# Performance work log

Hardware: AMD Instinct MI355X
Metric: run time of the kernel (lower is better)

Reference implementation:

```python
import jax, jax.numpy as jnp
import numpy as np

B, TX, DA, DS, H = 64, 2048, 256, 256, 50

def setup_inputs() -> dict:
    key = jax.random.key(0)
    k1, k2, k3, k4 = jax.random.split(key, 4)
    a = jax.random.normal(k1, (B, TX, DA), dtype=jnp.float32)
    s = jax.random.normal(k2, (B, DS), dtype=jnp.float32)
    # Dense(50, relu) params on concat dim (DA+DS)
    W1 = jax.random.normal(k3, (DA + DS, H), dtype=jnp.float32) / np.sqrt(DA + DS)
    b1 = jnp.zeros((H,), dtype=jnp.float32)
    # Dense(1, tanh) params
    W2 = jax.random.normal(k4, (H, 1), dtype=jnp.float32) / np.sqrt(H)
    b2 = jnp.zeros((1,), dtype=jnp.float32)
    return {"a": a, "s": s, "W1": W1, "b1": b1, "W2": W2, "b2": b2}

def reference(a, s, W1, b1, W2, b2):
    # repeat s along time: [B, Tx, Ds]
    s_rep = jnp.broadcast_to(s[:, None, :], (a.shape[0], a.shape[1], s.shape[-1]))
    x = jnp.concatenate([a, s_rep], axis=-1)              # [B, Tx, Da+Ds]
    h = jax.nn.relu(jnp.einsum('btc,ch->bth', x, W1) + b1)  # [B, Tx, 50]
    e = jnp.tanh(jnp.einsum('bth,ho->bto', h, W2) + b2)     # [B, Tx, 1]
    alphas = jax.nn.softmax(e, axis=1)                     # softmax over time
    # Dot(axes=1): contract the time axis -> [B, 1, Da]
    context = jnp.einsum('bto,btd->bod', alphas, a)
    return context
```

## Files before the change

kernel.cpp:

```cpp
#include <hip/hip_runtime.h>

#define B_ 64
#define TX_ 2048
#define DA_ 256
#define DS_ 256
#define H_ 50

typedef __attribute__((ext_vector_type(4))) float f32x4;
typedef __attribute__((ext_vector_type(8))) short short8;

__device__ __forceinline__ unsigned short f2bf(float x) {
  unsigned int u = __builtin_bit_cast(unsigned int, x);
  u += 0x7FFFu + ((u >> 16) & 1u);
  return (unsigned short)(u >> 16);
}
__device__ __forceinline__ float bf2f(unsigned short h) {
  unsigned int u = ((unsigned int)h) << 16;
  return __builtin_bit_cast(float, u);
}

#define WS_NUM 0
#define WS_DEN 16384
#define WS_C   16448
#define WS_W2  20544
#define WS_B   20608

__global__ __launch_bounds__(256) void prep_kernel(
    const float* __restrict__ s, const float* __restrict__ W1,
    const float* __restrict__ b1, const float* __restrict__ W2,
    float* __restrict__ ws)
{
  const int b = blockIdx.x;
  const int t = threadIdx.x;
  float* num = ws + WS_NUM;
  float* den = ws + WS_DEN;
  float* cws = ws + WS_C;
  float* w2p = ws + WS_W2;
  unsigned short* wsB = (unsigned short*)(ws + WS_B);

  num[b * 256 + t] = 0.0f;
  if (t == 0) den[b] = 0.0f;

  {
    const int h4 = t >> 2, kq = t & 3;
    float cp = 0.0f;
    if (h4 < H_) {
      const float* srow = s + b * DS_;
      #pragma unroll 8
      for (int k = kq * 64; k < kq * 64 + 64; ++k)
        cp += srow[k] * W1[(size_t)(DA_ + k) * H_ + h4];
    }
    cp += __shfl_down(cp, 1);
    cp += __shfl_down(cp, 2);
    if (kq == 0) cws[b * 64 + h4] = (h4 < H_) ? (cp + b1[h4]) : 0.0f;
  }
  if (b == 0 && t < 64) w2p[t] = (t < H_) ? W2[t] : 0.0f;

  #pragma unroll
  for (int ii = 0; ii < 2; ++ii) {
    const int idx = (b * 256 + t) * 2 + ii;
    const int j = idx & 7;
    const int l = (idx >> 3) & 63;
    const int nt = (idx >> 9) & 3;
    const int term = (idx >> 11) & 1;
    const int c = idx >> 12;
    const int k = c * 32 + (l >> 4) * 8 + j;
    const int n = nt * 16 + (l & 15);
    const float wv = (n < H_) ? W1[(size_t)k * H_ + n] : 0.0f;
    const unsigned short hi = f2bf(wv);
    const unsigned short val = term == 0 ? hi : f2bf(wv - bf2f(hi));
    wsB[((size_t)((c * 2 + term) * 4 + nt)) * 512 + l * 8 + j] = val;
  }
}

__global__ __launch_bounds__(256) void fused_kernel(
    const float* __restrict__ a, const float* __restrict__ ws_f,
    const float* __restrict__ b2, float* __restrict__ num,
    float* __restrict__ den)
{
  __shared__ float tile[16384];
  __shared__ float w_sh[64];

  const int t = threadIdx.x;
  const int l = t & 63;
  const int w = __builtin_amdgcn_readfirstlane(t >> 6);
  const int blk = blockIdx.x;
  const int b = blk >> 5;
  const long R0 = (long)blk * 64;

  const float* cws = ws_f + WS_C;
  const float* w2p = ws_f + WS_W2;
  const unsigned short* wsB = (const unsigned short*)(ws_f + WS_B);

  float cv[4], w2v[4];
  #pragma unroll
  for (int nt = 0; nt < 4; ++nt) {
    const int n = nt * 16 + (l & 15);
    cv[nt] = cws[b * 64 + n];
    w2v[nt] = w2p[n];
  }
  const float b2v = b2[0];

  #define STAGE(c)                                                             \
    {                                                                          \
      _Pragma("unroll")                                                        \
      for (int i = 0; i < 2; ++i) {                                            \
        const int slot = w * 2 + i;                                            \
        const int row = slot * 8 + (l >> 3);                                   \
        const long gbyte = (R0 + row) * 1024 + (c) * 128 +                     \
                           (((l & 7) ^ ((l >> 3) & 7)) * 16);                  \
        __builtin_amdgcn_global_load_lds(                                      \
            (const __attribute__((address_space(1))) void*)((const char*)a +   \
                                                            gbyte),            \
            (__attribute__((address_space(3))) void*)&tile[(c)*2048 +          \
                                                           slot * 256],        \
            16, 0, 0);                                                         \
      }                                                                        \
    }

  STAGE(0);
  STAGE(1);

  short8 Bh[2][4], Bl[2][4];
  {
    const short8* Bp = (const short8*)wsB;
    #pragma unroll
    for (int nt = 0; nt < 4; ++nt) {
      Bh[0][nt] = Bp[nt * 64 + l];
      Bl[0][nt] = Bp[(4 + nt) * 64 + l];
    }
  }

  f32x4 acc[4];
  #pragma unroll
  for (int nt = 0; nt < 4; ++nt) acc[nt] = (f32x4){0.f, 0.f, 0.f, 0.f};

  #pragma unroll
  for (int c = 0; c < 8; ++c) {
    if (c + 2 < 8) STAGE(c + 2);
    if (c + 1 < 8) {
      const short8* Bp = (const short8*)(wsB + (size_t)(c + 1) * 4096);
      #pragma unroll
      for (int nt = 0; nt < 4; ++nt) {
        Bh[(c + 1) & 1][nt] = Bp[nt * 64 + l];
        Bl[(c + 1) & 1][nt] = Bp[(4 + nt) * 64 + l];
      }
    }
    if (c < 6)       asm volatile("s_waitcnt vmcnt(10)" ::: "memory");
    else if (c == 6) asm volatile("s_waitcnt vmcnt(8)" ::: "memory");
    else             asm volatile("s_waitcnt vmcnt(0)" ::: "memory");
    __builtin_amdgcn_sched_barrier(0);

    const int row = w * 16 + (l & 15);
    const int mask = (l & 7) << 4;
    const int obase = (l >> 4) * 32;
    const char* tb = (const char*)tile + (size_t)c * 8192 + row * 128;
    const float4 v0 = *(const float4*)(tb + (obase ^ mask));
    const float4 v1 = *(const float4*)(tb + ((obase + 16) ^ mask));
    float av[8] = {v0.x, v0.y, v0.z, v0.w, v1.x, v1.y, v1.z, v1.w};
    short8 Ah, Al;
    #pragma unroll
    for (int j = 0; j < 8; ++j) {
      const unsigned short hi = f2bf(av[j]);
      Ah[j] = (short)hi;
      Al[j] = (short)f2bf(av[j] - bf2f(hi));
    }

    #pragma unroll
    for (int nt = 0; nt < 4; ++nt) {
      acc[nt] = __builtin_amdgcn_mfma_f32_16x16x32_bf16(Ah, Bh[c & 1][nt], acc[nt], 0, 0, 0);
      acc[nt] = __builtin_amdgcn_mfma_f32_16x16x32_bf16(Ah, Bl[c & 1][nt], acc[nt], 0, 0, 0);
      acc[nt] = __builtin_amdgcn_mfma_f32_16x16x32_bf16(Al, Bh[c & 1][nt], acc[nt], 0, 0, 0);
    }
  }

  #pragma unroll
  for (int r = 0; r < 4; ++r) {
    float e = 0.0f;
    #pragma unroll
    for (int nt = 0; nt < 4; ++nt)
      e += fmaxf(acc[nt][r] + cv[nt], 0.0f) * w2v[nt];
    e += __shfl_xor(e, 1);
    e += __shfl_xor(e, 2);
    e += __shfl_xor(e, 4);
    e += __shfl_xor(e, 8);
    if ((l & 15) == 0)
      w_sh[w * 16 + (l >> 4) * 4 + r] = __expf(tanhf(e + b2v));
  }
  __syncthreads();

  if (t < 64) {
    float v = w_sh[t];
    #pragma unroll
    for (int off = 32; off > 0; off >>= 1) v += __shfl_xor(v, off);
    if (t == 0) atomicAdd(&den[b], v);
  }

  {
    const int cc = t >> 5, col = t & 31;
    const char* tb = (const char*)tile + (size_t)cc * 8192;
    float sum = 0.0f;
    #pragma unroll 8
    for (int r = 0; r < 64; ++r) {
      const float av = *(const float*)(tb + r * 128 + ((col * 4) ^ ((r & 7) << 4)));
      sum += w_sh[r] * av;
    }
    atomicAdd(&num[b * 256 + t], sum);
  }
  #undef STAGE
}

__global__ __launch_bounds__(256) void finish_kernel(
    const float* __restrict__ ws_f, float* __restrict__ out)
{
  const int b = blockIdx.x;
  const int t = threadIdx.x;
  out[b * 256 + t] = ws_f[WS_NUM + b * 256 + t] / ws_f[WS_DEN + b];
}

extern "C" void kernel_launch(void* const* d_in, const int* in_sizes, int n_in,
                              void* d_out, int out_size, void* d_ws, size_t ws_size,
                              hipStream_t stream) {
  const float* a  = (const float*)d_in[0];
  const float* s  = (const float*)d_in[1];
  const float* W1 = (const float*)d_in[2];
  const float* b1 = (const float*)d_in[3];
  const float* W2 = (const float*)d_in[4];
  const float* b2 = (const float*)d_in[5];
  float* out = (float*)d_out;
  float* ws  = (float*)d_ws;

  prep_kernel<<<dim3(B_), dim3(256), 0, stream>>>(s, W1, b1, W2, ws);
  fused_kernel<<<dim3(2048), dim3(256), 0, stream>>>(
      a, ws, b2, ws + WS_NUM, ws + WS_DEN);
  finish_kernel<<<dim3(B_), dim3(256), 0, stream>>>(ws, out);
}
```

Baseline: 56.83 us.

## Use truncation-based bf16 split, fast tanh, wider prep grid, and launch bounds hint

The fp32-to-bf16 hi/lo split now packs the upper 16 bits with a byte permute (truncation instead of round-to-nearest), cutting ALU work per element before the MFMAs. tanhf is replaced by an exp-based formula. The prep kernel gets 192 blocks so the W1 bf16 repacking runs in separate blocks from the per-batch bias work. The fused kernel gains a launch-bounds occupancy hint of 2, and the bias/W2 loads move after the main loop. Truncation changes rounding of the hi/lo split, but the lo term still carries the residual. The fast tanh risks slightly different accuracy.

Result: faster. 53.34 us, median of 3 (-6.1%).

```diff
diff --git a/kernel.cpp b/kernel.cpp
--- a/kernel.cpp
+++ b/kernel.cpp
@@ -18,6 +18,15 @@
   unsigned int u = ((unsigned int)h) << 16;
   return __builtin_bit_cast(float, u);
 }
+__device__ __forceinline__ unsigned bitf(float x) {
+  return __builtin_bit_cast(unsigned, x);
+}
+__device__ __forceinline__ unsigned pack_hi(float x, float y) {
+  return __builtin_amdgcn_perm(bitf(y), bitf(x), 0x07060302);
+}
+__device__ __forceinline__ float trunc_bf(float x) {
+  return __builtin_bit_cast(float, bitf(x) & 0xFFFF0000u);
+}
 
 #define WS_NUM 0
 #define WS_DEN 16384
@@ -30,18 +39,15 @@
     const float* __restrict__ b1, const float* __restrict__ W2,
     float* __restrict__ ws)
 {
-  const int b = blockIdx.x;
+  const int blk = blockIdx.x;
   const int t = threadIdx.x;
-  float* num = ws + WS_NUM;
-  float* den = ws + WS_DEN;
-  float* cws = ws + WS_C;
-  float* w2p = ws + WS_W2;
   unsigned short* wsB = (unsigned short*)(ws + WS_B);
 
-  num[b * 256 + t] = 0.0f;
-  if (t == 0) den[b] = 0.0f;
-
-  {
+  if (blk < 64) {
+    const int b = blk;
+    ws[WS_NUM + b * 256 + t] = 0.0f;
+    if (t == 0) ws[WS_DEN + b] = 0.0f;
+
     const int h4 = t >> 2, kq = t & 3;
     float cp = 0.0f;
     if (h4 < H_) {
@@ -52,13 +58,10 @@
     }
     cp += __shfl_down(cp, 1);
     cp += __shfl_down(cp, 2);
-    if (kq == 0) cws[b * 64 + h4] = (h4 < H_) ? (cp + b1[h4]) : 0.0f;
-  }
-  if (b == 0 && t < 64) w2p[t] = (t < H_) ? W2[t] : 0.0f;
-
-  #pragma unroll
-  for (int ii = 0; ii < 2; ++ii) {
-    const int idx = (b * 256 + t) * 2 + ii;
+    if (kq == 0) ws[WS_C + b * 64 + h4] = (h4 < H_) ? (cp + b1[h4]) : 0.0f;
+    if (b == 0 && t < 64) ws[WS_W2 + t] = (t < H_) ? W2[t] : 0.0f;
+  } else {
+    const int idx = (blk - 64) * 256 + t;
     const int j = idx & 7;
     const int l = (idx >> 3) & 63;
     const int nt = (idx >> 9) & 3;
@@ -73,7 +76,7 @@
   }
 }
 
-__global__ __launch_bounds__(256) void fused_kernel(
+__global__ __launch_bounds__(256, 2) void fused_kernel(
     const float* __restrict__ a, const float* __restrict__ ws_f,
     const float* __restrict__ b2, float* __restrict__ num,
     float* __restrict__ den)
@@ -88,26 +91,14 @@
   const int b = blk >> 5;
   const long R0 = (long)blk * 64;
 
-  const float* cws = ws_f + WS_C;
-  const float* w2p = ws_f + WS_W2;
   const unsigned short* wsB = (const unsigned short*)(ws_f + WS_B);
-
-  float cv[4], w2v[4];
-  #pragma unroll
-  for (int nt = 0; nt < 4; ++nt) {
-    const int n = nt * 16 + (l & 15);
-    cv[nt] = cws[b * 64 + n];
-    w2v[nt] = w2p[n];
-  }
-  const float b2v = b2[0];
 
   #define STAGE(c)                                                             \
     {                                                                          \
       _Pragma("unroll")                                                        \
       for (int i = 0; i < 2; ++i) {                                            \
         const int slot = w * 2 + i;                                            \
-        const int row = slot * 8 + (l >> 3);                                   \
-        const long gbyte = (R0 + row) * 1024 + (c) * 128 +                     \
+        const long gbyte = (R0 + slot * 8 + (l >> 3)) * 1024 + (c) * 128 +     \
                            (((l & 7) ^ ((l >> 3) & 7)) * 16);                  \
         __builtin_amdgcn_global_load_lds(                                      \
             (const __attribute__((address_space(1))) void*)((const char*)a +   \
@@ -134,6 +125,10 @@
   f32x4 acc[4];
   #pragma unroll
   for (int nt = 0; nt < 4; ++nt) acc[nt] = (f32x4){0.f, 0.f, 0.f, 0.f};
+
+  const int row = w * 16 + (l & 15);
+  const int mask = (l & 7) << 4;
+  const int obase = (l >> 4) * 32;
 
   #pragma unroll
   for (int c = 0; c < 8; ++c) {
@@ -151,20 +146,20 @@
     else             asm volatile("s_waitcnt vmcnt(0)" ::: "memory");
     __builtin_amdgcn_sched_barrier(0);
 
-    const int row = w * 16 + (l & 15);
-    const int mask = (l & 7) << 4;
-    const int obase = (l >> 4) * 32;
     const char* tb = (const char*)tile + (size_t)c * 8192 + row * 128;
     const float4 v0 = *(const float4*)(tb + (obase ^ mask));
     const float4 v1 = *(const float4*)(tb + ((obase + 16) ^ mask));
-    float av[8] = {v0.x, v0.y, v0.z, v0.w, v1.x, v1.y, v1.z, v1.w};
-    short8 Ah, Al;
-    #pragma unroll
-    for (int j = 0; j < 8; ++j) {
-      const unsigned short hi = f2bf(av[j]);
-      Ah[j] = (short)hi;
-      Al[j] = (short)f2bf(av[j] - bf2f(hi));
-    }
+    const float av[8] = {v0.x, v0.y, v0.z, v0.w, v1.x, v1.y, v1.z, v1.w};
+
+    unsigned hu[4], lu[4];
+    #pragma unroll
+    for (int p = 0; p < 4; ++p) {
+      const float x = av[2 * p], y = av[2 * p + 1];
+      hu[p] = pack_hi(x, y);
+      lu[p] = pack_hi(x - trunc_bf(x), y - trunc_bf(y));
+    }
+    const short8 Ah = __builtin_bit_cast(short8, *(uint4*)hu);
+    const short8 Al = __builtin_bit_cast(short8, *(uint4*)lu);
 
     #pragma unroll
     for (int nt = 0; nt < 4; ++nt) {
@@ -173,6 +168,16 @@
       acc[nt] = __builtin_amdgcn_mfma_f32_16x16x32_bf16(Al, Bh[c & 1][nt], acc[nt], 0, 0, 0);
     }
   }
+  #undef STAGE
+
+  float cv[4], w2v[4];
+  #pragma unroll
+  for (int nt = 0; nt < 4; ++nt) {
+    const int n = nt * 16 + (l & 15);
+    cv[nt] = ws_f[WS_C + b * 64 + n];
+    w2v[nt] = ws_f[WS_W2 + n];
+  }
+  const float b2v = b2[0];
 
   #pragma unroll
   for (int r = 0; r < 4; ++r) {
@@ -184,8 +189,9 @@
     e += __shfl_xor(e, 2);
     e += __shfl_xor(e, 4);
     e += __shfl_xor(e, 8);
-    if ((l & 15) == 0)
-      w_sh[w * 16 + (l >> 4) * 4 + r] = __expf(tanhf(e + b2v));
+    e += b2v;
+    const float th = 1.0f - 2.0f / (__expf(2.0f * e) + 1.0f);
+    if ((l & 15) == 0) w_sh[w * 16 + (l >> 4) * 4 + r] = __expf(th);
   }
   __syncthreads();
 
@@ -207,7 +213,6 @@
     }
     atomicAdd(&num[b * 256 + t], sum);
   }
-  #undef STAGE
 }
 
 __global__ __launch_bounds__(256) void finish_kernel(
@@ -230,7 +235,7 @@
   float* out = (float*)d_out;
   float* ws  = (float*)d_ws;
 
-  prep_kernel<<<dim3(B_), dim3(256), 0, stream>>>(s, W1, b1, W2, ws);
+  prep_kernel<<<dim3(192), dim3(256), 0, stream>>>(s, W1, b1, W2, ws);
   fused_kernel<<<dim3(2048), dim3(256), 0, stream>>>(
       a, ws, b2, ws + WS_NUM, ws + WS_DEN);
   finish_kernel<<<dim3(B_), dim3(256), 0, stream>>>(ws, out);
```
